# Kernel optimization log

Hardware: AMD Instinct MI355X
Metric: run time of the kernel (lower is better)

The kernel has to match this reference:

```python
import jax, jax.numpy as jnp
import numpy as np

EMB_DIM = 512
HIDDEN = 512
NODE_DIM = 256
NUM_NODES = 64
L_RNN = 3
BATCH = 2048


def setup_inputs() -> dict:
    key = jax.random.key(0)
    ks = jax.random.split(key, 8)
    s = 0.05

    def rn(k, shape):
        return jax.random.normal(k, shape, dtype=jnp.float32) * s

    return {
        "emb": jax.random.normal(ks[0], (BATCH, EMB_DIM), dtype=jnp.float32),
        "Win1": rn(ks[1], (HIDDEN, EMB_DIM)),
        "bin1": jnp.zeros((HIDDEN,), jnp.float32),
        "Win2": rn(ks[2], (L_RNN * HIDDEN, HIDDEN)),
        "bin2": jnp.zeros((L_RNN * HIDDEN,), jnp.float32),
        "Wih": rn(ks[3], (L_RNN, 4 * HIDDEN, HIDDEN)),
        "Whh": rn(ks[4], (L_RNN, 4 * HIDDEN, HIDDEN)),
        "bih": jnp.zeros((L_RNN, 4 * HIDDEN), jnp.float32),
        "bhh": jnp.zeros((L_RNN, 4 * HIDDEN), jnp.float32),
        "Wout1": rn(ks[5], (HIDDEN, HIDDEN)),
        "bout1": jnp.zeros((HIDDEN,), jnp.float32),
        "Wout2": rn(ks[6], (NODE_DIM, HIDDEN)),
        "bout2": jnp.zeros((NODE_DIM,), jnp.float32),
    }


def reference(emb, Win1, bin1, Win2, bin2, Wih, Whh, bih, bhh,
              Wout1, bout1, Wout2, bout2):
    B = emb.shape[0]
    # FNN_in: emb -> initial hidden states for all LSTM layers
    hx = jax.nn.relu(emb @ Win1.T + bin1) @ Win2.T + bin2      # [B, L*H]
    hx = hx.reshape(B, L_RNN, HIDDEN).transpose(1, 0, 2)        # [L, B, H]
    cx = jnp.zeros_like(hx)
    x0 = jnp.zeros((B, HIDDEN), dtype=emb.dtype)                # first input (zeros)

    def step(carry, _):
        h, c, x = carry
        hs, cs = [], []
        inp = x
        for l in range(L_RNN):  # small fixed layer loop
            g = inp @ Wih[l].T + bih[l] + h[l] @ Whh[l].T + bhh[l]  # [B, 4H]
            i, f, gg, o = jnp.split(g, 4, axis=-1)  # PyTorch gate order i,f,g,o
            c_new = jax.nn.sigmoid(f) * c[l] + jax.nn.sigmoid(i) * jnp.tanh(gg)
            h_new = jax.nn.sigmoid(o) * jnp.tanh(c_new)
            hs.append(h_new)
            cs.append(c_new)
            inp = h_new
        return (jnp.stack(hs), jnp.stack(cs), inp), inp

    _, ys = jax.lax.scan(step, (hx, cx, x0), None, length=NUM_NODES)  # [T, B, H]

    x = ys.transpose(1, 0, 2).reshape(B * NUM_NODES, HIDDEN)    # [B*T, H]
    x = jax.nn.relu(x @ Wout1.T + bout1) @ Wout2.T + bout2      # FNN_out
    return x.reshape(B, NUM_NODES, NODE_DIM)
```

## Files before the change

### kernel.cpp

```cpp
#include <hip/hip_runtime.h>
#include <hip/hip_bf16.h>
#include <cstdint>
#include <cstddef>

using bf16 = __hip_bfloat16;
typedef short bf16x8 __attribute__((ext_vector_type(8)));
typedef float f32x4 __attribute__((ext_vector_type(4)));

#define CHUNK 64

__device__ __forceinline__ float fsigmoid(float x) {
  return 1.0f / (1.0f + __expf(-x));
}
__device__ __forceinline__ float ftanh_(float x) {
  float e = __expf(-2.0f * fabsf(x));
  float t = (1.0f - e) / (1.0f + e);
  return copysignf(t, x);
}

__device__ __forceinline__ void gload_lds16(const void* g, void* l) {
  __builtin_amdgcn_global_load_lds(
      (const __attribute__((address_space(1))) void*)g,
      (__attribute__((address_space(3))) void*)l, 16, 0, 0);
}

__global__ void cvt_bf16_kernel(const float* __restrict__ in, bf16* __restrict__ out, int n) {
  int i = blockIdx.x * blockDim.x + threadIdx.x;
  int stride = gridDim.x * blockDim.x;
  for (; i < n; i += stride) out[i] = __float2bfloat16(in[i]);
}

__global__ void build_wf_kernel(const float* __restrict__ Wih, const float* __restrict__ Whh,
                                const float* __restrict__ bih, const float* __restrict__ bhh,
                                bf16* __restrict__ Wf, float* __restrict__ bfused) {
  int i = blockIdx.x * 256 + threadIdx.x;
  int k = i & 1023;
  int r = (i >> 10) & 2047;
  int l = i >> 21;
  int u = r >> 6, gate = (r >> 4) & 3, v = r & 15;
  int j = u * 16 + v;
  int srow = l * 2048 + gate * 512 + j;
  float val = (k < 512) ? Wih[(size_t)srow * 512 + k] : Whh[(size_t)srow * 512 + (k - 512)];
  Wf[i] = __float2bfloat16(val);
  if (k == 0) bfused[l * 2048 + r] = bih[srow] + bhh[srow];
}

template <int EPI>
__device__ __forceinline__ void epilogue(
    f32x4 (&acc)[2][4], int m0, int n0, int wr, int wc, int lane,
    const float* __restrict__ bias, void* out0, void* out1, void* out2,
    float* __restrict__ cst, int ldo, int aux) {
  const int l16 = lane & 15;
  const int rbase = (lane >> 4) * 4;

  if constexpr (EPI == 0) {
    bf16* O = (bf16*)out0;
#pragma unroll
    for (int mi = 0; mi < 2; ++mi)
#pragma unroll
      for (int ni = 0; ni < 4; ++ni) {
        int col = n0 + wc * 64 + ni * 16 + l16;
        float bvv = bias[col];
#pragma unroll
        for (int r = 0; r < 4; ++r) {
          int row = m0 + wr * 32 + mi * 16 + rbase + r;
          float v2 = acc[mi][ni][r] + bvv;
          O[(size_t)row * ldo + col] = __float2bfloat16(fmaxf(v2, 0.f));
        }
      }
  } else if constexpr (EPI == 2) {
#pragma unroll
    for (int mi = 0; mi < 2; ++mi)
#pragma unroll
      for (int ni = 0; ni < 4; ++ni) {
        int col = n0 + wc * 64 + ni * 16 + l16;
        int lyr = col >> 9;
        bf16* O = (bf16*)(lyr == 0 ? out0 : (lyr == 1 ? out1 : out2));
        int j = col & 511;
        float bvv = bias[col];
#pragma unroll
        for (int r = 0; r < 4; ++r) {
          int row = m0 + wr * 32 + mi * 16 + rbase + r;
          O[(size_t)row * 512 + j] = __float2bfloat16(acc[mi][ni][r] + bvv);
        }
      }
  } else if constexpr (EPI == 3) {
    bf16* H = (bf16*)out0;
    bf16* Y = (bf16*)out1;
    int ucol = ((n0 >> 6) + wc) * 16 + l16;
    float bi = bias[n0 + wc * 64 + 0 + l16];
    float bff = bias[n0 + wc * 64 + 16 + l16];
    float bg = bias[n0 + wc * 64 + 32 + l16];
    float bo = bias[n0 + wc * 64 + 48 + l16];
#pragma unroll
    for (int mi = 0; mi < 2; ++mi)
#pragma unroll
      for (int r = 0; r < 4; ++r) {
        int row = m0 + wr * 32 + mi * 16 + rbase + r;
        float gi = acc[mi][0][r] + bi;
        float gf = acc[mi][1][r] + bff;
        float gg = acc[mi][2][r] + bg;
        float go = acc[mi][3][r] + bo;
        size_t idx = (size_t)row * 512 + ucol;
        float cold = cst[idx];
        float cn = fsigmoid(gf) * cold + fsigmoid(gi) * ftanh_(gg);
        float hn = fsigmoid(go) * ftanh_(cn);
        cst[idx] = cn;
        bf16 hb = __float2bfloat16(hn);
        H[idx] = hb;
        if (Y) Y[((size_t)row * CHUNK + aux) * 512 + ucol] = hb;
      }
  } else if constexpr (EPI == 4) {
    float* O = (float*)out0;
#pragma unroll
    for (int mi = 0; mi < 2; ++mi)
#pragma unroll
      for (int ni = 0; ni < 4; ++ni) {
        int col = n0 + wc * 64 + ni * 16 + l16;
        float bvv = bias[col];
#pragma unroll
        for (int r = 0; r < 4; ++r) {
          int row = m0 + wr * 32 + mi * 16 + rbase + r;
          int orow = ((row / CHUNK) << 6) + aux + (row % CHUNK);
          O[(size_t)orow * ldo + col] = acc[mi][ni][r] + bvv;
        }
      }
  }
}

template <int EPI>
__global__ __launch_bounds__(512) void gemm_bt(
    const bf16* __restrict__ A0, const bf16* __restrict__ A1,
    const bf16* __restrict__ Bw, const float* __restrict__ bias,
    void* __restrict__ out0, void* __restrict__ out1, void* __restrict__ out2,
    float* __restrict__ cst,
    int K, int lda, int ldo, int aux) {
  const int tid = threadIdx.x;
  const int wave = tid >> 6;
  const int lane = tid & 63;

  const int gx = gridDim.x;
  const int nwg = gx * gridDim.y;
  const int flat = blockIdx.x + gx * blockIdx.y;
  int m0, n0;
  if (gx == 16 && gridDim.y == 16) {
    const int xcd = flat & 7;
    const int w = flat >> 3;
    const int mt = (xcd >> 2) * 8 + (w & 7);
    const int nt = (xcd & 3) * 4 + (w >> 3);
    m0 = mt * 128;
    n0 = nt * 128;
  } else {
    const int v = (flat & 7) * (nwg >> 3) + (flat >> 3);
    m0 = (v % gx) * 128;
    n0 = (v / gx) * 128;
  }

  const int wr = wave >> 1, wc = wave & 1;

  __shared__ alignas(16) short ls[4 * 16384];
  char* lsb = (char*)ls;

  f32x4 acc[2][4];
#pragma unroll
  for (int i = 0; i < 2; ++i)
#pragma unroll
    for (int j = 0; j < 4; ++j) acc[i][j] = (f32x4){0.f, 0.f, 0.f, 0.f};

  const int s_row = tid >> 3;
  const int s_k = (((tid & 7) ^ ((tid >> 3) & 7)) * 8);
  const int l16 = lane & 15;
  const int khi = lane >> 4;
  const int sx = l16 & 7;

  const int nk = K >> 6;

  auto stage_half = [&](int step, int half) {
    int b = step & 3;
    int kt = step << 6;
    char* base = lsb + b * 32768;
    if (half == 0) {
      const bf16* as = A0;
      int kk = kt;
      if (kt >= 512) { as = A1; kk = kt - 512; }
      gload_lds16(as + (size_t)(m0 + s_row) * lda + kk + s_k, base + tid * 16);
      gload_lds16(as + (size_t)(m0 + 64 + s_row) * lda + kk + s_k, base + 8192 + tid * 16);
    } else {
      gload_lds16(Bw + (size_t)(n0 + s_row) * K + kt + s_k, base + 16384 + tid * 16);
      gload_lds16(Bw + (size_t)(n0 + 64 + s_row) * K + kt + s_k, base + 24576 + tid * 16);
    }
  };

  auto compute_half = [&](int step, int kk) {
    int b = step & 3;
    const short* LA = ls + b * 16384;
    const short* LB = LA + 8192;
    bf16x8 af[2], bv[4];
    int pgA = ((kk * 4 + khi) ^ sx) * 8;
#pragma unroll
    for (int i = 0; i < 2; ++i)
      af[i] = *(const bf16x8*)&LA[(wr * 32 + i * 16 + l16) * 64 + pgA];
#pragma unroll
    for (int i = 0; i < 4; ++i)
      bv[i] = *(const bf16x8*)&LB[(wc * 64 + i * 16 + l16) * 64 + pgA];
    __builtin_amdgcn_s_setprio(1);
#pragma unroll
    for (int mi = 0; mi < 2; ++mi)
#pragma unroll
      for (int ni = 0; ni < 4; ++ni)
        acc[mi][ni] = __builtin_amdgcn_mfma_f32_16x16x32_bf16(af[mi], bv[ni], acc[mi][ni], 0, 0, 0);
    __builtin_amdgcn_s_setprio(0);
  };

  stage_half(0, 0); stage_half(0, 1);
  stage_half(1, 0); stage_half(1, 1);
  for (int t = 0; t < nk - 2; ++t) {
    asm volatile("s_waitcnt vmcnt(4)" ::: "memory");
    __builtin_amdgcn_s_barrier();
    __builtin_amdgcn_sched_barrier(0);
    compute_half(t, 0);
    stage_half(t + 2, 0);
    compute_half(t, 1);
    stage_half(t + 2, 1);
  }
  asm volatile("s_waitcnt vmcnt(4)" ::: "memory");
  __builtin_amdgcn_s_barrier();
  __builtin_amdgcn_sched_barrier(0);
  compute_half(nk - 2, 0);
  compute_half(nk - 2, 1);
  asm volatile("s_waitcnt vmcnt(0)" ::: "memory");
  __builtin_amdgcn_s_barrier();
  __builtin_amdgcn_sched_barrier(0);
  compute_half(nk - 1, 0);
  compute_half(nk - 1, 1);

  epilogue<EPI>(acc, m0, n0, wr, wc, lane, bias, out0, out1, out2, cst, ldo, aux);
}

template <int EPI>
__global__ __launch_bounds__(512) void gemm2(
    const bf16* __restrict__ A0,
    const bf16* __restrict__ Bw, const float* __restrict__ bias,
    void* __restrict__ out0, float* __restrict__ cst,
    int K, int lda, int ldo, int aux) {
  const int tid = threadIdx.x;
  const int wave = tid >> 6;
  const int lane = tid & 63;

  const int gx = gridDim.x;
  const int nwg = gx * gridDim.y;
  const int flat = blockIdx.x + gx * blockIdx.y;
  const int v = (flat & 7) * (nwg >> 3) + (flat >> 3);
  const int m0 = (v % gx) * 128;
  const int n0 = (v / gx) * 128;

  const int wr = wave >> 1, wc = wave & 1;

  __shared__ alignas(16) short ls[2 * 16384];
  char* lsb = (char*)ls;

  f32x4 acc[2][4];
#pragma unroll
  for (int i = 0; i < 2; ++i)
#pragma unroll
    for (int j = 0; j < 4; ++j) acc[i][j] = (f32x4){0.f, 0.f, 0.f, 0.f};

  const int s_row = tid >> 3;
  const int s_k = (((tid & 7) ^ ((tid >> 3) & 7)) * 8);
  const int l16 = lane & 15;
  const int khi = lane >> 4;
  const int sx = l16 & 7;

  const int nk = K >> 6;

  auto stage = [&](int step) {
    int b = step & 1;
    int kt = step << 6;
    char* base = lsb + b * 32768;
    gload_lds16(A0 + (size_t)(m0 + s_row) * lda + kt + s_k, base + tid * 16);
    gload_lds16(A0 + (size_t)(m0 + 64 + s_row) * lda + kt + s_k, base + 8192 + tid * 16);
    gload_lds16(Bw + (size_t)(n0 + s_row) * K + kt + s_k, base + 16384 + tid * 16);
    gload_lds16(Bw + (size_t)(n0 + 64 + s_row) * K + kt + s_k, base + 24576 + tid * 16);
  };

  auto compute = [&](int step) {
    int b = step & 1;
    const short* LA = ls + b * 16384;
    const short* LB = LA + 8192;
    bf16x8 af[2][2], bv[4][2];
#pragma unroll
    for (int kk = 0; kk < 2; ++kk) {
      int pgA = ((kk * 4 + khi) ^ sx) * 8;
#pragma unroll
      for (int i = 0; i < 2; ++i)
        af[i][kk] = *(const bf16x8*)&LA[(wr * 32 + i * 16 + l16) * 64 + pgA];
#pragma unroll
      for (int i = 0; i < 4; ++i)
        bv[i][kk] = *(const bf16x8*)&LB[(wc * 64 + i * 16 + l16) * 64 + pgA];
    }
    __builtin_amdgcn_s_setprio(1);
#pragma unroll
    for (int kk = 0; kk < 2; ++kk)
#pragma unroll
      for (int mi = 0; mi < 2; ++mi)
#pragma unroll
        for (int ni = 0; ni < 4; ++ni)
          acc[mi][ni] = __builtin_amdgcn_mfma_f32_16x16x32_bf16(af[mi][kk], bv[ni][kk], acc[mi][ni], 0, 0, 0);
    __builtin_amdgcn_s_setprio(0);
  };

  stage(0);
  for (int t = 0; t < nk; ++t) {
    asm volatile("s_waitcnt vmcnt(0)" ::: "memory");
    __builtin_amdgcn_s_barrier();
    __builtin_amdgcn_sched_barrier(0);
    if (t + 1 < nk) stage(t + 1);
    compute(t);
  }

  epilogue<EPI>(acc, m0, n0, wr, wc, lane, bias, out0, nullptr, nullptr, cst, ldo, aux);
}

extern "C" void kernel_launch(void* const* d_in, const int* in_sizes, int n_in,
                              void* d_out, int out_size, void* d_ws, size_t ws_size,
                              hipStream_t stream) {
  const float* emb = (const float*)d_in[0];
  const float* Win1 = (const float*)d_in[1];
  const float* bin1 = (const float*)d_in[2];
  const float* Win2 = (const float*)d_in[3];
  const float* bin2 = (const float*)d_in[4];
  const float* Wih = (const float*)d_in[5];
  const float* Whh = (const float*)d_in[6];
  const float* bih = (const float*)d_in[7];
  const float* bhh = (const float*)d_in[8];
  const float* Wout1 = (const float*)d_in[9];
  const float* bout1 = (const float*)d_in[10];
  const float* Wout2 = (const float*)d_in[11];
  const float* bout2 = (const float*)d_in[12];
  float* out = (float*)d_out;
  (void)in_sizes; (void)n_in; (void)out_size; (void)ws_size;

  char* p = (char*)d_ws;
  auto carve = [&](size_t bytes) {
    char* r = p;
    p += (bytes + 255) & ~(size_t)255;
    return r;
  };

  bf16* Wf = (bf16*)carve((size_t)3 * 2048 * 1024 * 2);
  float* bfuse = (float*)carve((size_t)3 * 2048 * 4);
  bf16* Win1b = (bf16*)carve((size_t)512 * 512 * 2);
  bf16* Win2b = (bf16*)carve((size_t)1536 * 512 * 2);
  bf16* Wout1b = (bf16*)carve((size_t)512 * 512 * 2);
  bf16* Wout2b = (bf16*)carve((size_t)256 * 512 * 2);
  bf16* embb = (bf16*)carve((size_t)2048 * 512 * 2);
  bf16* C1 = (bf16*)carve((size_t)2048 * 512 * 2);
  bf16* hbuf = (bf16*)carve((size_t)2 * 3 * 2048 * 512 * 2);
  float* cst = (float*)carve((size_t)3 * 2048 * 512 * 4);
  bf16* x0 = (bf16*)carve((size_t)2048 * 512 * 2);
  bf16* ysc = (bf16*)carve((size_t)2048 * CHUNK * 512 * 2);
  bf16* Z = (bf16*)carve((size_t)2048 * CHUNK * 512 * 2);

  hipMemsetAsync(cst, 0, (size_t)3 * 2048 * 512 * 4, stream);
  hipMemsetAsync(x0, 0, (size_t)2048 * 512 * 2, stream);

  cvt_bf16_kernel<<<1024, 256, 0, stream>>>(emb, embb, 2048 * 512);
  cvt_bf16_kernel<<<1024, 256, 0, stream>>>(Win1, Win1b, 512 * 512);
  cvt_bf16_kernel<<<1024, 256, 0, stream>>>(Win2, Win2b, 1536 * 512);
  cvt_bf16_kernel<<<1024, 256, 0, stream>>>(Wout1, Wout1b, 512 * 512);
  cvt_bf16_kernel<<<512, 256, 0, stream>>>(Wout2, Wout2b, 256 * 512);
  build_wf_kernel<<<(3 * 2048 * 1024) / 256, 256, 0, stream>>>(Wih, Whh, bih, bhh, Wf, bfuse);

  auto hset = [&](int s, int l) { return hbuf + ((size_t)s * 3 + l) * 2048 * 512; };

  gemm_bt<0><<<dim3(16, 4), 512, 0, stream>>>(embb, nullptr, Win1b, bin1,
                                              C1, nullptr, nullptr, nullptr, 512, 512, 512, 0);
  gemm_bt<2><<<dim3(16, 12), 512, 0, stream>>>(C1, nullptr, Win2b, bin2,
                                               hset(0, 0), hset(0, 1), hset(0, 2), nullptr,
                                               512, 512, 0, 0);

  for (int t = 0; t < 64; ++t) {
    int cur = t & 1;
    bf16* hR0 = hset(cur, 0);
    bf16* hR1 = hset(cur, 1);
    bf16* hR2 = hset(cur, 2);
    bf16* hW0 = hset(cur ^ 1, 0);
    bf16* hW1 = hset(cur ^ 1, 1);
    bf16* hW2 = hset(cur ^ 1, 2);
    const bf16* inp0 = (t == 0) ? (const bf16*)x0 : (const bf16*)hR2;
    int tc = t % CHUNK;

    gemm_bt<3><<<dim3(16, 16), 512, 0, stream>>>(inp0, hR0, Wf, bfuse,
                                                 hW0, nullptr, nullptr, cst,
                                                 1024, 512, 0, tc);
    gemm_bt<3><<<dim3(16, 16), 512, 0, stream>>>(hW0, hR1, Wf + (size_t)2048 * 1024, bfuse + 2048,
                                                 hW1, nullptr, nullptr, cst + (size_t)2048 * 512,
                                                 1024, 512, 0, tc);
    gemm_bt<3><<<dim3(16, 16), 512, 0, stream>>>(hW1, hR2, Wf + (size_t)2 * 2048 * 1024, bfuse + 2 * 2048,
                                                 hW2, ysc, nullptr, cst + (size_t)2 * 2048 * 512,
                                                 1024, 512, 0, tc);

    if (tc == CHUNK - 1) {
      gemm2<0><<<dim3(2048 * CHUNK / 128, 4), 512, 0, stream>>>(
          ysc, Wout1b, bout1, Z, nullptr, 512, 512, 512, 0);
      gemm2<4><<<dim3(2048 * CHUNK / 128, 2), 512, 0, stream>>>(
          Z, Wout2b, bout2, out, nullptr, 512, 512, 256, t - (CHUNK - 1));
    }
  }
}
```

Before: 2.998 ms.

## Deepen gemm2 pipeline to 4-stage K=32 ring and remap tiles per XCD

gemm2 now stages K in 32-wide slices into a 4-buffer LDS ring and keeps two loads in flight ahead of compute, using partial vmcnt waits in place of a full drain each iteration. The swizzle is adjusted for 32-element rows. The workgroup-to-tile mapping now gives each XCD a contiguous band of M rows and iterates N within it, for better L2 reuse of A. Smaller K steps mean twice as many barriers per tile. The new mapping also assumes gridDim.x is divisible by 8.

```diff
diff --git a/kernel.cpp b/kernel.cpp
--- a/kernel.cpp
+++ b/kernel.cpp
@@ -248,15 +248,17 @@
   const int lane = tid & 63;
 
   const int gx = gridDim.x;
-  const int nwg = gx * gridDim.y;
+  const int nY = gridDim.y;
   const int flat = blockIdx.x + gx * blockIdx.y;
-  const int v = (flat & 7) * (nwg >> 3) + (flat >> 3);
-  const int m0 = (v % gx) * 128;
-  const int n0 = (v / gx) * 128;
+  const int xcd = flat & 7;
+  const int seq = flat >> 3;
+  const int mpx = gx >> 3;
+  const int m0 = (xcd * mpx + seq / nY) * 128;
+  const int n0 = (seq % nY) * 128;
 
   const int wr = wave >> 1, wc = wave & 1;
 
-  __shared__ alignas(16) short ls[2 * 16384];
+  __shared__ alignas(16) short ls[4 * 8192];
   char* lsb = (char*)ls;
 
   f32x4 acc[2][4];
@@ -265,58 +267,58 @@
 #pragma unroll
     for (int j = 0; j < 4; ++j) acc[i][j] = (f32x4){0.f, 0.f, 0.f, 0.f};
 
-  const int s_row = tid >> 3;
-  const int s_k = (((tid & 7) ^ ((tid >> 3) & 7)) * 8);
+  const int s_row = tid >> 2;
+  const int s_k = (((tid & 3) ^ ((tid >> 3) & 3)) * 8);
   const int l16 = lane & 15;
-  const int khi = lane >> 4;
-  const int sx = l16 & 7;
-
-  const int nk = K >> 6;
+  const int sw = (((lane >> 4) ^ ((l16 >> 1) & 3)) << 3);
+
+  const int nk = K >> 5;
 
   auto stage = [&](int step) {
-    int b = step & 1;
-    int kt = step << 6;
-    char* base = lsb + b * 32768;
+    int b = step & 3;
+    int kt = step << 5;
+    char* base = lsb + b * 16384;
     gload_lds16(A0 + (size_t)(m0 + s_row) * lda + kt + s_k, base + tid * 16);
-    gload_lds16(A0 + (size_t)(m0 + 64 + s_row) * lda + kt + s_k, base + 8192 + tid * 16);
-    gload_lds16(Bw + (size_t)(n0 + s_row) * K + kt + s_k, base + 16384 + tid * 16);
-    gload_lds16(Bw + (size_t)(n0 + 64 + s_row) * K + kt + s_k, base + 24576 + tid * 16);
+    gload_lds16(Bw + (size_t)(n0 + s_row) * K + kt + s_k, base + 8192 + tid * 16);
   };
 
   auto compute = [&](int step) {
-    int b = step & 1;
-    const short* LA = ls + b * 16384;
-    const short* LB = LA + 8192;
-    bf16x8 af[2][2], bv[4][2];
-#pragma unroll
-    for (int kk = 0; kk < 2; ++kk) {
-      int pgA = ((kk * 4 + khi) ^ sx) * 8;
-#pragma unroll
-      for (int i = 0; i < 2; ++i)
-        af[i][kk] = *(const bf16x8*)&LA[(wr * 32 + i * 16 + l16) * 64 + pgA];
-#pragma unroll
-      for (int i = 0; i < 4; ++i)
-        bv[i][kk] = *(const bf16x8*)&LB[(wc * 64 + i * 16 + l16) * 64 + pgA];
-    }
+    int b = step & 3;
+    const short* LA = ls + b * 8192;
+    const short* LB = LA + 4096;
+    bf16x8 af[2], bv[4];
+#pragma unroll
+    for (int i = 0; i < 2; ++i)
+      af[i] = *(const bf16x8*)&LA[(wr * 32 + i * 16 + l16) * 32 + sw];
+#pragma unroll
+    for (int i = 0; i < 4; ++i)
+      bv[i] = *(const bf16x8*)&LB[(wc * 64 + i * 16 + l16) * 32 + sw];
     __builtin_amdgcn_s_setprio(1);
 #pragma unroll
-    for (int kk = 0; kk < 2; ++kk)
-#pragma unroll
-      for (int mi = 0; mi < 2; ++mi)
-#pragma unroll
-        for (int ni = 0; ni < 4; ++ni)
-          acc[mi][ni] = __builtin_amdgcn_mfma_f32_16x16x32_bf16(af[mi][kk], bv[ni][kk], acc[mi][ni], 0, 0, 0);
+    for (int mi = 0; mi < 2; ++mi)
+#pragma unroll
+      for (int ni = 0; ni < 4; ++ni)
+        acc[mi][ni] = __builtin_amdgcn_mfma_f32_16x16x32_bf16(af[mi], bv[ni], acc[mi][ni], 0, 0, 0);
     __builtin_amdgcn_s_setprio(0);
   };
 
   stage(0);
-  for (int t = 0; t < nk; ++t) {
-    asm volatile("s_waitcnt vmcnt(0)" ::: "memory");
+  stage(1);
+  for (int t = 0; t < nk - 2; ++t) {
+    stage(t + 2);
+    asm volatile("s_waitcnt vmcnt(4)" ::: "memory");
     __builtin_amdgcn_s_barrier();
     __builtin_amdgcn_sched_barrier(0);
-    if (t + 1 < nk) stage(t + 1);
     compute(t);
   }
+  asm volatile("s_waitcnt vmcnt(2)" ::: "memory");
+  __builtin_amdgcn_s_barrier();
+  __builtin_amdgcn_sched_barrier(0);
+  compute(nk - 2);
+  asm volatile("s_waitcnt vmcnt(0)" ::: "memory");
+  __builtin_amdgcn_s_barrier();
+  __builtin_amdgcn_sched_barrier(0);
+  compute(nk - 1);
 
   epilogue<EPI>(acc, m0, n0, wr, wc, lane, bias, out0, nullptr, nullptr, cst, ldo, aux);
 }
```

Result: no change. 2.985 ms (-0.5%).
